# Kernel tuning notes

Measured on AMD Instinct MI355X. Metric: run time of the kernel, lower is better.

## Reference

```python
import jax, jax.numpy as jnp
import numpy as np

B, I, H = 1024, 128, 512  # batch, input_size, hidden_size


def setup_inputs() -> dict:
    key = jax.random.key(0)
    ks = jax.random.split(key, 9)
    lim_w = np.sqrt(6.0 / (2 * H * 2 * I + H))          # xavier_uniform gain=1
    fan_in, fan_out = 2 * H * 2 * I, H                  # per _calculate_fan_in_and_fan_out on [H,2H,2I]
    lim_b = np.sqrt(3.0 / (0.5 * (fan_in + fan_out)))
    lim_m = np.sqrt(6.0 / (2 * H + H))
    return {
        "in0": jax.random.normal(ks[0], (B, I), jnp.float32),
        "in1": jax.random.normal(ks[1], (B, I), jnp.float32),
        "s0": jax.random.normal(ks[2], (B, H), jnp.float32),
        "s1": jax.random.normal(ks[3], (B, H), jnp.float32),
        "W1": jax.random.uniform(ks[4], (H, 2 * H, 2 * I), jnp.float32, -lim_w, lim_w),
        "b1": jax.random.uniform(ks[5], (H,), jnp.float32, -lim_b, lim_b),
        "W2": jax.random.uniform(ks[6], (H, 2 * H, 2 * I), jnp.float32, -lim_w, lim_w),
        "b2": jax.random.uniform(ks[7], (H,), jnp.float32, -lim_b, lim_b),
        "Wmerge": jax.random.uniform(ks[8], (2 * H, H), jnp.float32, -lim_m, lim_m),
    }


def reference(in0, in1, s0, s1, W1, b1, W2, b2, Wmerge):
    h = jnp.concatenate([s0, s1], axis=1)   # [B, 2H]
    x = jnp.concatenate([in0, in1], axis=1) # [B, 2I]
    # Bilinear contraction: equivalent to outer-product [B,2H,2I] reduced by W [H,2H,2I],
    # expressed without materializing the outer product.
    m1 = jnp.einsum('bj,bk,ljk->bl', h, x, W1)  # [B, H]
    m2 = jnp.einsum('bj,bk,ljk->bl', h, x, W2)  # [B, H]
    state_tilda = jnp.tanh(m1 + b1)
    u = jax.nn.sigmoid(m2 + b2)
    new_state = u * state_tilda + (1.0 - u) * (h @ Wmerge)
    return new_state  # original returns (output, new_state) which are the same array
```

## Files before the change

kernel.cpp:

```cpp
#include <hip/hip_runtime.h>
#include <hip/hip_bf16.h>


typedef __attribute__((ext_vector_type(8))) short short8;
typedef __attribute__((ext_vector_type(4))) float f32x4;
typedef __attribute__((ext_vector_type(2))) float f32x2;
typedef unsigned short ushort_t;

__device__ __forceinline__ unsigned cvtpk(float a, float b) {
  unsigned r;
  asm("v_cvt_pk_bf16_f32 %0, %1, %2" : "=v"(r) : "v"(a), "v"(b));
  return r;
}

__device__ __forceinline__ f32x2 pkmul(f32x2 a, f32x2 b) {
  f32x2 r;
  asm("v_pk_mul_f32 %0, %1, %2" : "=v"(r) : "v"(a), "v"(b));
  return r;
}

__device__ __forceinline__ ushort_t f2bu(float f) {
  __hip_bfloat16 b = __float2bfloat16(f);
  union { __hip_bfloat16 b; ushort_t u; } cv;
  cv.b = b;
  return cv.u;
}

__global__ void prep_k(const float* __restrict__ in0, const float* __restrict__ in1,
                       const float* __restrict__ s0, const float* __restrict__ s1,
                       const float* __restrict__ Wm,
                       ushort_t* __restrict__ hb, ushort_t* __restrict__ xb,
                       ushort_t* __restrict__ WmT) {
  __shared__ float tl[64][65];
  const int bid = blockIdx.x, t = threadIdx.x;
  if (bid < 256) {
#pragma unroll
    for (int i = 0; i < 4; ++i) {
      int e = bid * 4096 + i * 1024 + t * 4;
      int b = e >> 10, j = e & 1023;
      const float* src = (j < 512) ? (s0 + (size_t)b * 512 + j)
                                   : (s1 + (size_t)b * 512 + j - 512);
      float4 v = *(const float4*)src;
      ushort4 o;
      o.x = f2bu(v.x); o.y = f2bu(v.y); o.z = f2bu(v.z); o.w = f2bu(v.w);
      *(ushort4*)(hb + e) = o;
    }
  } else if (bid < 272) {
#pragma unroll
    for (int i = 0; i < 16; ++i) {
      int e = (bid - 256) * 16384 + i * 1024 + t * 4;
      int b = e >> 8, kx = e & 255;
      const float* src = (kx < 128) ? (in0 + (size_t)b * 128 + kx)
                                    : (in1 + (size_t)b * 128 + kx - 128);
      float4 v = *(const float4*)src;
      ushort4 o;
      o.x = f2bu(v.x); o.y = f2bu(v.y); o.z = f2bu(v.z); o.w = f2bu(v.w);
      *(ushort4*)(xb + e) = o;
    }
  } else {
    int q = bid - 272;
    int j0 = (q >> 3) * 64;
    int l0 = (q & 7) * 64;
#pragma unroll
    for (int i = 0; i < 16; ++i) {
      int idx = i * 256 + t; int r = idx >> 6, c = idx & 63;
      tl[r][c] = Wm[(size_t)(j0 + r) * 512 + l0 + c];
    }
    __syncthreads();
#pragma unroll
    for (int i = 0; i < 16; ++i) {
      int idx = i * 256 + t; int r = idx >> 6, c = idx & 63;
      WmT[(size_t)(l0 + r) * 1024 + j0 + c] = f2bu(tl[c][r]);
    }
  }
}

__global__ __launch_bounds__(1024)
__attribute__((amdgpu_waves_per_eu(4, 4))) void bilin_k(
    const float* __restrict__ W1, const float* __restrict__ W2,
    const ushort_t* __restrict__ hb, const ushort_t* __restrict__ xb,
    float* __restrict__ accg) {
  __shared__ uint4 smemv[5376];

  const int ntile = blockIdx.x;
  const int chunk = blockIdx.y;
  const int kxwin = (chunk & 7) * 32;
  const int jbase0 = (chunk >> 3) * 512;
  const int tid = threadIdx.x;
  const int wave = tid >> 6;
  const int lane = tid & 63;
  const int l15 = lane & 15;
  const int lg = lane >> 4;
  const int wrow = wave * 64;

  const int scol = tid >> 5;
  const int sj = (tid & 31) >> 2;
  const int sc4 = tid & 3;
  const int wbyte = scol * 512 + ((sj * 64 + sc4 * 16) ^ ((scol & 7) << 4));

  const float* Wsel = (ntile < 16) ? W1 : W2;
  const float* gW = Wsel + (size_t)(ntile & 15) * 32 * 262144 +
                    (size_t)scol * 262144 + (size_t)(jbase0 + sj) * 256 +
                    kxwin + sc4 * 8;

  f32x2 xf[4][4];
#pragma unroll
  for (int g = 0; g < 4; ++g) {
    uint4 xw = *(const uint4*)(xb + (size_t)(wrow + g * 16 + l15) * 256 + kxwin + lg * 8);
    unsigned w[4] = {xw.x, xw.y, xw.z, xw.w};
#pragma unroll
    for (int p = 0; p < 4; ++p) {
      xf[g][p][0] = __uint_as_float(w[p] << 16);
      xf[g][p][1] = __uint_as_float(w[p] & 0xFFFF0000u);
    }
  }

  f32x4 acc[4][2];
  const f32x4 z4 = {0.f, 0.f, 0.f, 0.f};
#pragma unroll
  for (int g = 0; g < 4; ++g)
#pragma unroll
    for (int nc = 0; nc < 2; ++nc) acc[g][nc] = z4;

  {
    float4 wa = *(const float4*)gW;
    float4 wb = *(const float4*)(gW + 4);
    uint4 pk;
    pk.x = cvtpk(wa.x, wa.y); pk.y = cvtpk(wa.z, wa.w);
    pk.z = cvtpk(wb.x, wb.y); pk.w = cvtpk(wb.z, wb.w);
    *(uint4*)((char*)smemv + wbyte) = pk;
  }
  __syncthreads();

  int cur = 0;
  for (int t = 0; t < 64; ++t) {
    const int nxt = cur ^ 1;
    float4 wa, wb;
    if (t < 63) {
      const float* gp = gW + (size_t)(t + 1) * 2048;
      wa = *(const float4*)gp;
      wb = *(const float4*)(gp + 4);
    }

    const int jw = jbase0 + t * 8;
    uint4 hc[4];
#pragma unroll
    for (int g = 0; g < 4; ++g)
      hc[g] = *(const uint4*)(hb + (size_t)(wrow + g * 16 + l15) * 1024 + jw);

    const char* rb = (const char*)smemv + cur * 16384;

    short8 bfr[2][2];
#pragma unroll
    for (int nc = 0; nc < 2; ++nc) {
      int col = nc * 16 + l15;
      int byte = col * 512 + ((lg * 16) ^ ((col & 7) << 4));
      bfr[0][nc] = *(const short8*)(rb + byte);
    }

#pragma unroll
    for (int js = 0; js < 8; ++js) {
      const int pb = js & 1, nb = pb ^ 1;
      if (js < 7) {
#pragma unroll
        for (int nc = 0; nc < 2; ++nc) {
          int col = nc * 16 + l15;
          int byte = col * 512 + (((js + 1) * 64 + lg * 16) ^ ((col & 7) << 4));
          bfr[nb][nc] = *(const short8*)(rb + byte);
        }
      }
      __builtin_amdgcn_s_setprio(1);
#pragma unroll
      for (int g = 0; g < 4; ++g) {
        unsigned hwrd = (js < 2) ? hc[g].x : (js < 4) ? hc[g].y
                       : (js < 6) ? hc[g].z : hc[g].w;
        float hf = __uint_as_float((js & 1) ? (hwrd & 0xFFFF0000u) : (hwrd << 16));
        f32x2 hf2; hf2[0] = hf; hf2[1] = hf;
        union { unsigned u[4]; short8 s; } av;
#pragma unroll
        for (int p = 0; p < 4; ++p) {
          f32x2 m = pkmul(xf[g][p], hf2);
          av.u[p] = cvtpk(m[0], m[1]);
        }
        short8 afr = av.s;
#pragma unroll
        for (int nc = 0; nc < 2; ++nc)
          acc[g][nc] = __builtin_amdgcn_mfma_f32_16x16x32_bf16(
              afr, bfr[pb][nc], acc[g][nc], 0, 0, 0);
      }
      __builtin_amdgcn_s_setprio(0);
    }

    if (t < 63) {
      uint4 pk;
      pk.x = cvtpk(wa.x, wa.y); pk.y = cvtpk(wa.z, wa.w);
      pk.z = cvtpk(wb.x, wb.y); pk.w = cvtpk(wb.z, wb.w);
      *(uint4*)((char*)smemv + nxt * 16384 + wbyte) = pk;
    }
    __syncthreads();
    cur = nxt;
  }

#pragma unroll
  for (int g = 0; g < 4; ++g)
#pragma unroll
    for (int nc = 0; nc < 2; ++nc)
#pragma unroll
      for (int r = 0; r < 4; ++r) {
        int b = wrow + g * 16 + lg * 4 + r;
        int n = ntile * 32 + nc * 16 + l15;
        unsafeAtomicAdd(&accg[(size_t)b * 1024 + n], acc[g][nc][r]);
      }
}

__device__ __forceinline__ short8 ld8bf(const ushort_t* p) {
  union { uint4 v; short8 s; } cv;
  cv.v = *(const uint4*)p;
  return cv.s;
}

__global__ __launch_bounds__(256) void merge_k(const ushort_t* __restrict__ hb,
                                               const ushort_t* __restrict__ WmT,
                                               float* __restrict__ mout) {
  const int tid = threadIdx.x;
  const int wave = tid >> 6, lane = tid & 63;
  const int l15 = lane & 15, lg = lane >> 4;
  const int m0 = blockIdx.x * 64 + (wave >> 1) * 32;
  const int n0 = blockIdx.y * 64 + (wave & 1) * 32;
  const f32x4 z4 = {0.f, 0.f, 0.f, 0.f};
  f32x4 acc[2][2];
#pragma unroll
  for (int g = 0; g < 2; ++g)
#pragma unroll
    for (int nc = 0; nc < 2; ++nc) acc[g][nc] = z4;

  for (int k = 0; k < 1024; k += 32) {
    short8 af[2], bf[2];
#pragma unroll
    for (int g = 0; g < 2; ++g)
      af[g] = ld8bf(hb + (size_t)(m0 + g * 16 + l15) * 1024 + k + lg * 8);
#pragma unroll
    for (int nc = 0; nc < 2; ++nc)
      bf[nc] = ld8bf(WmT + (size_t)(n0 + nc * 16 + l15) * 1024 + k + lg * 8);
#pragma unroll
    for (int g = 0; g < 2; ++g)
#pragma unroll
      for (int nc = 0; nc < 2; ++nc)
        acc[g][nc] = __builtin_amdgcn_mfma_f32_16x16x32_bf16(
            af[g], bf[nc], acc[g][nc], 0, 0, 0);
  }
#pragma unroll
  for (int g = 0; g < 2; ++g)
#pragma unroll
    for (int nc = 0; nc < 2; ++nc)
#pragma unroll
      for (int r = 0; r < 4; ++r)
        mout[(size_t)(m0 + g * 16 + lg * 4 + r) * 512 + n0 + nc * 16 + l15] =
            acc[g][nc][r];
}

__global__ void fin_k(const float* __restrict__ accg, const float* __restrict__ mout,
                      const float* __restrict__ b1, const float* __restrict__ b2,
                      float* __restrict__ out) {
  int idx = blockIdx.x * 256 + threadIdx.x;
  int b = idx >> 9, l = idx & 511;
  float m1 = accg[(size_t)b * 1024 + l];
  float m2 = accg[(size_t)b * 1024 + 512 + l];
  float st = tanhf(m1 + b1[l]);
  float u = 1.f / (1.f + expf(-(m2 + b2[l])));
  out[idx] = u * st + (1.f - u) * mout[idx];
}

extern "C" void kernel_launch(void* const* d_in, const int* in_sizes, int n_in,
                              void* d_out, int out_size, void* d_ws, size_t ws_size,
                              hipStream_t stream) {
  const float* in0 = (const float*)d_in[0];
  const float* in1 = (const float*)d_in[1];
  const float* s0  = (const float*)d_in[2];
  const float* s1  = (const float*)d_in[3];
  const float* W1  = (const float*)d_in[4];
  const float* b1  = (const float*)d_in[5];
  const float* W2  = (const float*)d_in[6];
  const float* b2  = (const float*)d_in[7];
  const float* Wm  = (const float*)d_in[8];
  float* out = (float*)d_out;

  char* ws = (char*)d_ws;
  float*    accg = (float*)(ws + 0);
  float*    mout = (float*)(ws + (4u << 20));
  ushort_t* hb   = (ushort_t*)(ws + (6u << 20));
  ushort_t* xb   = (ushort_t*)(ws + (8u << 20));
  ushort_t* WmT  = (ushort_t*)(ws + (8u << 20) + (512u << 10));

  hipMemsetAsync(accg, 0, 4u << 20, stream);
  prep_k<<<400, 256, 0, stream>>>(in0, in1, s0, s1, Wm, hb, xb, WmT);
  bilin_k<<<dim3(32, 16), 1024, 0, stream>>>(W1, W2, hb, xb, accg);
  merge_k<<<dim3(16, 8), 256, 0, stream>>>(hb, WmT, mout);
  fin_k<<<2048, 256, 0, stream>>>(accg, mout, b1, b2, out);
}
```

Before: 797.2 us.

## Split bilinear kernel batch into halves with 512-thread blocks and staged W loads

```diff
diff --git a/kernel.cpp b/kernel.cpp
--- a/kernel.cpp
+++ b/kernel.cpp
@@ -75,15 +75,16 @@
   }
 }
 
-__global__ __launch_bounds__(1024)
+__global__ __launch_bounds__(512)
 __attribute__((amdgpu_waves_per_eu(4, 4))) void bilin_k(
     const float* __restrict__ W1, const float* __restrict__ W2,
     const ushort_t* __restrict__ hb, const ushort_t* __restrict__ xb,
     float* __restrict__ accg) {
-  __shared__ uint4 smemv[5376];
+  __shared__ uint4 smemv[3584];
 
   const int ntile = blockIdx.x;
   const int chunk = blockIdx.y;
+  const int mhalf = blockIdx.z;
   const int kxwin = (chunk & 7) * 32;
   const int jbase0 = (chunk >> 3) * 512;
   const int tid = threadIdx.x;
@@ -91,17 +92,16 @@
   const int lane = tid & 63;
   const int l15 = lane & 15;
   const int lg = lane >> 4;
-  const int wrow = wave * 64;
-
-  const int scol = tid >> 5;
-  const int sj = (tid & 31) >> 2;
+  const int wrow = mhalf * 512 + wave * 64;
+
+  const int scol = tid >> 4;
+  const int sj2 = (tid >> 2) & 3;
   const int sc4 = tid & 3;
-  const int wbyte = scol * 512 + ((sj * 64 + sc4 * 16) ^ ((scol & 7) << 4));
+  const int swzw = (scol & 7) << 4;
 
   const float* Wsel = (ntile < 16) ? W1 : W2;
-  const float* gW = Wsel + (size_t)(ntile & 15) * 32 * 262144 +
-                    (size_t)scol * 262144 + (size_t)(jbase0 + sj) * 256 +
-                    kxwin + sc4 * 8;
+  const float* gW = Wsel + (size_t)((ntile & 15) * 32 + scol) * 262144 +
+                    (size_t)(jbase0 + sj2) * 256 + kxwin + sc4 * 8;
 
   f32x2 xf[4][4];
 #pragma unroll
@@ -122,12 +122,15 @@
 #pragma unroll
     for (int nc = 0; nc < 2; ++nc) acc[g][nc] = z4;
 
-  {
-    float4 wa = *(const float4*)gW;
-    float4 wb = *(const float4*)(gW + 4);
+#pragma unroll
+  for (int sub = 0; sub < 2; ++sub) {
+    const float* gp = gW + sub * 1024;
+    float4 wa = *(const float4*)gp;
+    float4 wb = *(const float4*)(gp + 4);
     uint4 pk;
     pk.x = cvtpk(wa.x, wa.y); pk.y = cvtpk(wa.z, wa.w);
     pk.z = cvtpk(wb.x, wb.y); pk.w = cvtpk(wb.z, wb.w);
+    int wbyte = scol * 512 + ((((sub * 4 + sj2) * 64) + sc4 * 16) ^ swzw);
     *(uint4*)((char*)smemv + wbyte) = pk;
   }
   __syncthreads();
@@ -135,6 +138,9 @@
   int cur = 0;
   for (int t = 0; t < 64; ++t) {
     const int nxt = cur ^ 1;
+    const char* rb = (const char*)smemv + cur * 16384;
+    const int jw = jbase0 + t * 8;
+
     float4 wa, wb;
     if (t < 63) {
       const float* gp = gW + (size_t)(t + 1) * 2048;
@@ -142,13 +148,10 @@
       wb = *(const float4*)(gp + 4);
     }
 
-    const int jw = jbase0 + t * 8;
     uint4 hc[4];
 #pragma unroll
     for (int g = 0; g < 4; ++g)
       hc[g] = *(const uint4*)(hb + (size_t)(wrow + g * 16 + l15) * 1024 + jw);
-
-    const char* rb = (const char*)smemv + cur * 16384;
 
     short8 bfr[2][2];
 #pragma unroll
@@ -189,12 +192,24 @@
               afr, bfr[pb][nc], acc[g][nc], 0, 0, 0);
       }
       __builtin_amdgcn_s_setprio(0);
+
+      if (js == 3 && t < 63) {
+        uint4 pk;
+        pk.x = cvtpk(wa.x, wa.y); pk.y = cvtpk(wa.z, wa.w);
+        pk.z = cvtpk(wb.x, wb.y); pk.w = cvtpk(wb.z, wb.w);
+        int wbyte = scol * 512 + (((sj2 * 64) + sc4 * 16) ^ swzw);
+        *(uint4*)((char*)smemv + nxt * 16384 + wbyte) = pk;
+        const float* gp = gW + (size_t)(t + 1) * 2048 + 1024;
+        wa = *(const float4*)gp;
+        wb = *(const float4*)(gp + 4);
+      }
     }
 
     if (t < 63) {
       uint4 pk;
       pk.x = cvtpk(wa.x, wa.y); pk.y = cvtpk(wa.z, wa.w);
       pk.z = cvtpk(wb.x, wb.y); pk.w = cvtpk(wb.z, wb.w);
+      int wbyte = scol * 512 + ((((4 + sj2) * 64) + sc4 * 16) ^ swzw);
       *(uint4*)((char*)smemv + nxt * 16384 + wbyte) = pk;
     }
     __syncthreads();
@@ -294,7 +309,7 @@
 
   hipMemsetAsync(accg, 0, 4u << 20, stream);
   prep_k<<<400, 256, 0, stream>>>(in0, in1, s0, s1, Wm, hb, xb, WmT);
-  bilin_k<<<dim3(32, 16), 1024, 0, stream>>>(W1, W2, hb, xb, accg);
+  bilin_k<<<dim3(32, 16, 2), 512, 0, stream>>>(W1, W2, hb, xb, accg);
   merge_k<<<dim3(16, 8), 256, 0, stream>>>(hb, WmT, mout);
   fin_k<<<2048, 256, 0, stream>>>(accg, mout, b1, b2, out);
 }
```

After: 1.360 ms. 1.71x slower.
